# Optimization experiments

Hardware: AMD Instinct MI355X
Metric: run time of the kernel (lower is better)

The kernel has to match this reference:

```python
import jax, jax.numpy as jnp
import numpy as np

B, F, H, W = 1, 6, 20, 26
S = F * H * W            # 3120 tokens
DIM, NH, HD = 1536, 12, 128
C = HD // 2              # 64 rotary channels
T_C = C - 2 * (C // 3)   # 22 temporal channels
H_C = C // 3             # 21
W_C = C // 3             # 21
LOCAL_FRAMES = 4         # local_attn_size (in frames)
SINK_FRAMES = 1          # sink_size (in frames)
EPS = 1e-6
MAX_POS = 1024


def _angle_table(n_ch):
    inv = 1.0 / (10000.0 ** (np.arange(n_ch, dtype=np.float64) / n_ch))
    return np.outer(np.arange(MAX_POS, dtype=np.float64), inv)


def setup_inputs() -> dict:
    key = jax.random.key(0)
    ks = jax.random.split(key, 8)
    sc = 0.02
    ang = np.concatenate([_angle_table(T_C), _angle_table(H_C), _angle_table(W_C)], axis=1)  # [1024, 64]
    return {
        "x": jax.random.normal(ks[0], (B, S, DIM), jnp.float32),
        "seq_lens": jnp.array([S], jnp.int32),
        "grid_sizes": jnp.array([[F, H, W]], jnp.int32),
        "freqs_cos": jnp.asarray(np.cos(ang), jnp.float32),
        "freqs_sin": jnp.asarray(np.sin(ang), jnp.float32),
        "Wq": jax.random.normal(ks[1], (DIM, DIM), jnp.float32) * sc,
        "bq": jnp.zeros((DIM,), jnp.float32),
        "Wk": jax.random.normal(ks[2], (DIM, DIM), jnp.float32) * sc,
        "bk": jnp.zeros((DIM,), jnp.float32),
        "Wv": jax.random.normal(ks[3], (DIM, DIM), jnp.float32) * sc,
        "bv": jnp.zeros((DIM,), jnp.float32),
        "Wo": jax.random.normal(ks[4], (DIM, DIM), jnp.float32) * sc,
        "bo": jnp.zeros((DIM,), jnp.float32),
        "gq": jnp.ones((DIM,), jnp.float32),
        "gk": jnp.ones((DIM,), jnp.float32),
    }


def _rms_norm(x, g):
    # WanRMSNorm: x * rsqrt(mean(x^2) + eps) * weight
    return x * jax.lax.rsqrt(jnp.mean(x * x, axis=-1, keepdims=True) + EPS) * g


def _rope_apply(x, freqs_cos, freqs_sin):
    # x: [B, S, NH, HD]; per-token 3D (f,h,w) rotary on consecutive pairs.
    pos = jnp.arange(S)
    f = pos // (H * W)
    hh = (pos // W) % H
    ww = pos % W
    cos_t, cos_h, cos_w = freqs_cos[:, :T_C], freqs_cos[:, T_C:T_C + H_C], freqs_cos[:, T_C + H_C:]
    sin_t, sin_h, sin_w = freqs_sin[:, :T_C], freqs_sin[:, T_C:T_C + H_C], freqs_sin[:, T_C + H_C:]
    cos = jnp.concatenate([cos_t[f], cos_h[hh], cos_w[ww]], axis=-1)[None, :, None, :]  # [1,S,1,C]
    sin = jnp.concatenate([sin_t[f], sin_h[hh], sin_w[ww]], axis=-1)[None, :, None, :]
    xp = x.reshape(B, S, NH, C, 2)
    xr, xi = xp[..., 0], xp[..., 1]
    out = jnp.stack([xr * cos - xi * sin, xr * sin + xi * cos], axis=-1)
    return out.reshape(B, S, NH, HD)


def _block_mask():
    # frame-causal + local window (in frames) + sink frames: [S, S] bool
    fid = jnp.arange(S) // (H * W)
    fi, fj = fid[:, None], fid[None, :]
    return (fj <= fi) & ((fi - fj < LOCAL_FRAMES) | (fj < SINK_FRAMES))


def reference(x, seq_lens, grid_sizes, freqs_cos, freqs_sin,
              Wq, bq, Wk, bk, Wv, bv, Wo, bo, gq, gk):
    q = _rms_norm(x @ Wq + bq, gq).reshape(B, S, NH, HD)
    k = _rms_norm(x @ Wk + bk, gk).reshape(B, S, NH, HD)
    v = (x @ Wv + bv).reshape(B, S, NH, HD)
    rq = _rope_apply(q, freqs_cos, freqs_sin)
    rk = _rope_apply(k, freqs_cos, freqs_sin)
    scale = 1.0 / jnp.sqrt(jnp.asarray(HD, x.dtype))
    scores = jnp.einsum('bind,bjnd->bnij', rq, rk) * scale  # [B,NH,S,S]
    scores = jnp.where(_block_mask()[None, None], scores, jnp.finfo(scores.dtype).min)
    attn = jax.nn.softmax(scores, axis=-1)
    out = jnp.einsum('bnij,bjnd->bind', attn, v).reshape(B, S, DIM)
    return out @ Wo + bo
```

## Files before the change

kernel.cpp:

```cpp
#include <hip/hip_runtime.h>
#include <hip/hip_bf16.h>
#include <stdint.h>

typedef short v8s __attribute__((ext_vector_type(8)));
typedef float v4f __attribute__((ext_vector_type(4)));
typedef unsigned short u16;

#define S_LEN 3120
#define DIMN 1536
#define NHEAD 12
#define HDIM 128
#define FRM 520
#define NT64 49
#define T64_PH 166
#define TOT64 1992
#define NSTEP32 17
#define SCALE_QK 0.088388347648318447f
#define MAXOFF 12.0f

__device__ __forceinline__ v4f mfma16(v8s a, v8s b, v4f c) {
  return __builtin_amdgcn_mfma_f32_16x16x32_bf16(a, b, c, 0, 0, 0);
}
__device__ __forceinline__ float b2f(u16 u) {
  union { float f; unsigned int i; } x; x.i = ((unsigned int)u) << 16; return x.f;
}
__device__ __forceinline__ u16 f2b(float f) {
  union { float f; unsigned int i; } x; x.f = f;
  unsigned int r = x.i + 0x7FFFu + ((x.i >> 16) & 1u);
  return (u16)(r >> 16);
}
__device__ __forceinline__ void async16(const void* g, void* l) {
  __builtin_amdgcn_global_load_lds(
      (__attribute__((address_space(1))) const void*)g,
      (__attribute__((address_space(3))) void*)l, 16, 0, 0);
}

__global__ void detect_dtype(const u16* __restrict__ w, int* __restrict__ flag) {
  __shared__ int sh;
  int t = threadIdx.x;
  if (t == 0) sh = 0;
  __syncthreads();
  u16 m0 = (u16)(w[2 * t] & 0x7FFF);
  u16 m1 = (u16)(w[2 * t + 1] & 0x7FFF);
  if (m0 >= 0x4480 || m1 >= 0x4480) atomicOr(&sh, 1);
  __syncthreads();
  if (t == 0) *flag = sh;
}

struct PrepArgs {
  const void* tin[4]; u16* tout[4];
  const void* csrc[9]; u16* cdst[9]; int cn[9];
};
__global__ __launch_bounds__(256) void prep(PrepArgs a, const int* __restrict__ flag) {
  int isf = *flag;
  int z = blockIdx.z;
  int t = threadIdx.x;
  if (z < 4) {
    __shared__ u16 tile[32][33];
    const float* inf = (const float*)a.tin[z];
    const u16* inb = (const u16*)a.tin[z];
    u16* out = a.tout[z];
    int tx = t & 31, ty = t >> 5;
    int gr0 = blockIdx.y * 32, gc0 = blockIdx.x * 32;
#pragma unroll
    for (int i = 0; i < 4; ++i) {
      int r = ty + i * 8;
      size_t idx = (size_t)(gr0 + r) * DIMN + gc0 + tx;
      tile[r][tx] = isf ? f2b(inf[idx]) : inb[idx];
    }
    __syncthreads();
#pragma unroll
    for (int i = 0; i < 4; ++i) {
      int r = ty + i * 8;
      out[(size_t)(gc0 + r) * DIMN + gr0 + tx] = tile[tx][r];
    }
  } else {
    int id = z - 4;
    int n = a.cn[id];
    const float* sf = (const float*)a.csrc[id];
    const u16* sb = (const u16*)a.csrc[id];
    u16* d = a.cdst[id];
    int bidx = blockIdx.y * gridDim.x + blockIdx.x;
    int stride = gridDim.x * gridDim.y * 256;
    for (int i = bidx * 256 + t; i < n; i += stride)
      d[i] = isf ? f2b(sf[i]) : sb[i];
  }
}

__global__ __launch_bounds__(256) void transpose16(const u16* __restrict__ in,
                                                   u16* __restrict__ out,
                                                   int rows, int cols) {
  __shared__ u16 tile[32][33];
  int t = threadIdx.x;
  int tx = t & 31, ty = t >> 5;
  int gr0 = blockIdx.y * 32, gc0 = blockIdx.x * 32;
#pragma unroll
  for (int i = 0; i < 4; ++i) {
    int r = ty + i * 8;
    int gr = gr0 + r, gc = gc0 + tx;
    if (gr < rows && gc < cols) tile[r][tx] = in[(size_t)gr * cols + gc];
  }
  __syncthreads();
#pragma unroll
  for (int i = 0; i < 4; ++i) {
    int r = ty + i * 8;
    int orow = gc0 + r, ocol = gr0 + tx;
    if (orow < cols && ocol < rows) out[(size_t)orow * rows + ocol] = tile[tx][r];
  }
}

template <int MT>
__global__ __launch_bounds__(256) void gemm3(
    const u16* __restrict__ A,
    const u16* BT0, const u16* BT1, const u16* BT2,
    const u16* b0, const u16* b1, const u16* b2,
    void* C0, void* C1, void* C2, int M, const int* __restrict__ flag, int dyn) {
  const u16* BT; const u16* bias; void* C;
  if (blockIdx.z == 0)      { BT = BT0; bias = b0; C = C0; }
  else if (blockIdx.z == 1) { BT = BT1; bias = b1; C = C1; }
  else                      { BT = BT2; bias = b2; C = C2; }
  int f32out = dyn ? *flag : 0;
  __shared__ __align__(16) short As[MT * 64];
  __shared__ __align__(16) short Bs[128 * 64];
  int t = threadIdx.x, w = t >> 6, l = t & 63;
  int ln = l & 15, lg = l >> 4;
  int m0 = blockIdx.y * MT, n0 = blockIdx.x * 128;
  int lr = l >> 3;
  int gl = (l & 7) ^ lr;
  constexpr int ACH = MT / 32;
  const u16* gAp[ACH]; short* lAp[ACH];
#pragma unroll
  for (int i = 0; i < ACH; ++i) {
    int c = w * ACH + i;
    int arow = min(m0 + c * 8 + lr, M - 1);
    gAp[i] = A + (size_t)arow * DIMN + gl * 8;
    lAp[i] = As + c * 512;
  }
  const u16* gBp[4]; short* lBp[4];
#pragma unroll
  for (int i = 0; i < 4; ++i) {
    int c = w * 4 + i;
    int brow = n0 + c * 8 + lr;
    gBp[i] = BT + (size_t)brow * DIMN + gl * 8;
    lBp[i] = Bs + c * 512;
  }
  constexpr int NJ = (MT == 128) ? 4 : 2;
  int wm = (MT == 128) ? (w & 1) : 0;
  int wn = (MT == 128) ? (w >> 1) : w;
  int aoff[2][4], boff[2][NJ];
#pragma unroll
  for (int ks = 0; ks < 2; ++ks) {
#pragma unroll
    for (int i = 0; i < 4; ++i) {
      int ar = wm * 64 + i * 16 + ln;
      aoff[ks][i] = ar * 64 + (((ks * 4 + lg) ^ (ar & 7)) * 8);
    }
#pragma unroll
    for (int j = 0; j < NJ; ++j) {
      int br = wn * (NJ * 16) + j * 16 + ln;
      boff[ks][j] = br * 64 + (((ks * 4 + lg) ^ (br & 7)) * 8);
    }
  }
  v4f acc[4][NJ] = {};
  for (int k0 = 0; k0 < DIMN; k0 += 64) {
    __syncthreads();
#pragma unroll
    for (int i = 0; i < ACH; ++i) async16(gAp[i] + k0, lAp[i]);
#pragma unroll
    for (int i = 0; i < 4; ++i) async16(gBp[i] + k0, lBp[i]);
    __syncthreads();
#pragma unroll
    for (int ks = 0; ks < 2; ++ks) {
      v8s af[4], bfr[NJ];
#pragma unroll
      for (int i = 0; i < 4; ++i) af[i] = *(const v8s*)(As + aoff[ks][i]);
#pragma unroll
      for (int j = 0; j < NJ; ++j) bfr[j] = *(const v8s*)(Bs + boff[ks][j]);
#pragma unroll
      for (int i = 0; i < 4; ++i)
#pragma unroll
        for (int j = 0; j < NJ; ++j) acc[i][j] = mfma16(af[i], bfr[j], acc[i][j]);
    }
  }
#pragma unroll
  for (int i = 0; i < 4; ++i) {
    int rb = m0 + wm * 64 + i * 16 + lg * 4;
#pragma unroll
    for (int j = 0; j < NJ; ++j) {
      int col = n0 + wn * (NJ * 16) + j * 16 + ln;
      float bv = b2f(bias[col]);
#pragma unroll
      for (int r = 0; r < 4; ++r) {
        int grow = rb + r;
        if (grow < M) {
          size_t idx = (size_t)grow * DIMN + col;
          float val = acc[i][j][r] + bv;
          if (f32out) ((float*)C)[idx] = val;
          else        ((u16*)C)[idx] = f2b(val);
        }
      }
    }
  }
}

__global__ __launch_bounds__(256) void norm_rope(u16* __restrict__ Q, u16* __restrict__ K,
                                                 const u16* __restrict__ gq,
                                                 const u16* __restrict__ gk,
                                                 const u16* __restrict__ fcos,
                                                 const u16* __restrict__ fsin) {
  int s = blockIdx.x;
  u16* base = (blockIdx.y == 0 ? Q : K) + (size_t)s * DIMN;
  const u16* g = (blockIdx.y == 0) ? gq : gk;
  int t = threadIdx.x;
  int e = t * 6;
  float x[6];
#pragma unroll
  for (int i = 0; i < 6; ++i) x[i] = b2f(base[e + i]);
  float ss = 0.f;
#pragma unroll
  for (int i = 0; i < 6; ++i) ss += x[i] * x[i];
#pragma unroll
  for (int off = 32; off > 0; off >>= 1) ss += __shfl_xor(ss, off);
  __shared__ float red[4];
  if ((t & 63) == 0) red[t >> 6] = ss;
  __syncthreads();
  float tot = red[0] + red[1] + red[2] + red[3];
  float rs = rsqrtf(tot * (1.0f / DIMN) + 1e-6f);
  int f = s / FRM;
  int hh = (s / 26) % 20;
  int ww = s % 26;
#pragma unroll
  for (int u = 0; u < 3; ++u) {
    int e0 = e + 2 * u;
    int c = (e0 & 127) >> 1;
    int p = (c < 22) ? f : ((c < 43) ? hh : ww);
    float co = b2f(fcos[p * 64 + c]);
    float si = b2f(fsin[p * 64 + c]);
    float xr = x[2 * u] * rs * b2f(g[e0]);
    float xi = x[2 * u + 1] * rs * b2f(g[e0 + 1]);
    base[e0]     = f2b(xr * co - xi * si);
    base[e0 + 1] = f2b(xr * si + xi * co);
  }
}

__global__ __launch_bounds__(128) void attn_block(const u16* __restrict__ Q,
                                                  const u16* __restrict__ K,
                                                  const u16* __restrict__ VT,
                                                  u16* __restrict__ Po,
                                                  float* __restrict__ Pl) {
  __shared__ __align__(16) short Ks[32 * 128];
  __shared__ __align__(16) short Vs[128 * 32];
  __shared__ __align__(16) short Pt[2][32 * 40];
  int t = threadIdx.x, w = t >> 6, l = t & 63;
  int ln = l & 15, lg = l >> 4;
  int task = blockIdx.x;
  int head = task / T64_PH, tid = task % T64_PH;
  int tile = 0, frame = 0;
  {
    int acc = 0;
    for (tile = 0; tile < NT64; ++tile) {
      int q0t = tile * 64;
      int f_lo = q0t / FRM;
      int f_hi = min(q0t + 63, S_LEN - 1) / FRM;
      int fstart = max(0, f_lo - 3);
      int sink = fstart > 0;
      int nf = f_hi - fstart + 1 + sink;
      if (tid < acc + nf) {
        int c = tid - acc;
        frame = sink ? (c == 0 ? 0 : fstart + c - 1) : (fstart + c);
        break;
      }
      acc += nf;
    }
  }
  int q0 = tile * 64 + w * 32;
  v8s qf[2][4];
  bool rowok[2][4];
#pragma unroll
  for (int g = 0; g < 2; ++g) {
    int row = min(q0 + g * 16 + ln, S_LEN - 1);
    const u16* qp = Q + (size_t)row * DIMN + head * HDIM + lg * 8;
#pragma unroll
    for (int c = 0; c < 4; ++c) qf[g][c] = *(const v8s*)(qp + c * 32);
#pragma unroll
    for (int r = 0; r < 4; ++r) {
      int qr = q0 + g * 16 + lg * 4 + r;
      int fi = (qr < S_LEN) ? qr / FRM : -1;
      rowok[g][r] = (frame <= fi) && ((fi - frame) < 4 || frame == 0);
    }
  }
  float lsum[2][4] = {};
  v4f o[2][8] = {};
  int kbeg = frame * FRM, kend = kbeg + FRM;
  int kr_i[4], kgl_i[4], vd_i[4], vgl_i[4];
#pragma unroll
  for (int i = 0; i < 4; ++i) {
    int n = (w * 4 + i) * 64 + l;
    kr_i[i] = n >> 4;
    kgl_i[i] = (n & 15) ^ (kr_i[i] & 15);
    vd_i[i] = n >> 2;
    vgl_i[i] = (n & 3) ^ (vd_i[i] & 3);
  }
  const u16* Kb = K + head * HDIM;
  for (int it = 0; it < NSTEP32; ++it) {
    int kb = kbeg + it * 32;
    __syncthreads();
#pragma unroll
    for (int i = 0; i < 4; ++i) {
      int krow = min(kb + kr_i[i], S_LEN - 1);
      async16(Kb + (size_t)krow * DIMN + kgl_i[i] * 8,
              (char*)Ks + (size_t)(w * 4 + i) * 1024);
      async16(VT + (size_t)(head * HDIM + vd_i[i]) * S_LEN + kb + vgl_i[i] * 8,
              (char*)Vs + (size_t)(w * 4 + i) * 1024);
    }
    __syncthreads();
    v4f s[2][2] = {};
#pragma unroll
    for (int kg = 0; kg < 2; ++kg) {
#pragma unroll
      for (int c = 0; c < 4; ++c) {
        v8s kf = *(const v8s*)(&Ks[(kg * 16 + ln) * 128 + (((c * 4 + lg) ^ ln) * 8)]);
        s[0][kg] = mfma16(qf[0][c], kf, s[0][kg]);
        s[1][kg] = mfma16(qf[1][c], kf, s[1][kg]);
      }
    }
#pragma unroll
    for (int g = 0; g < 2; ++g)
#pragma unroll
      for (int kg = 0; kg < 2; ++kg) {
        bool jv = (kb + kg * 16 + ln) < kend;
#pragma unroll
        for (int r = 0; r < 4; ++r) {
          float p = (rowok[g][r] && jv) ? __expf(s[g][kg][r] * SCALE_QK - MAXOFF) : 0.f;
          unsigned int bi = __float_as_uint(p) & 0xffff0000u;
          lsum[g][r] += __uint_as_float(bi);
          Pt[w][(g * 16 + lg * 4 + r) * 40 + kg * 16 + ln] = (u16)(bi >> 16);
        }
      }
    v8s pf0 = *(const v8s*)(&Pt[w][ln * 40 + lg * 8]);
    v8s pf1 = *(const v8s*)(&Pt[w][(16 + ln) * 40 + lg * 8]);
#pragma unroll
    for (int d = 0; d < 8; ++d) {
      int rr = d * 16 + ln;
      v8s vf = *(const v8s*)(&Vs[rr * 32 + ((lg ^ (rr & 3)) * 8)]);
      o[0][d] = mfma16(pf0, vf, o[0][d]);
      o[1][d] = mfma16(pf1, vf, o[1][d]);
    }
  }
#pragma unroll
  for (int g = 0; g < 2; ++g)
#pragma unroll
    for (int r = 0; r < 4; ++r) {
      float v = lsum[g][r];
      v += __shfl_xor(v, 1);
      v += __shfl_xor(v, 2);
      v += __shfl_xor(v, 4);
      v += __shfl_xor(v, 8);
      lsum[g][r] = v;
    }
  size_t pbase = (size_t)task * (64 * 128);
#pragma unroll
  for (int g = 0; g < 2; ++g)
#pragma unroll
    for (int d = 0; d < 8; ++d)
#pragma unroll
      for (int r = 0; r < 4; ++r) {
        int lrow = w * 32 + g * 16 + lg * 4 + r;
        Po[pbase + lrow * 128 + d * 16 + ln] = f2b(o[g][d][r]);
      }
  if (ln == 0) {
#pragma unroll
    for (int g = 0; g < 2; ++g)
#pragma unroll
      for (int r = 0; r < 4; ++r)
        Pl[task * 64 + w * 32 + g * 16 + lg * 4 + r] = lsum[g][r];
  }
}

__global__ __launch_bounds__(256) void attn_combine(const u16* __restrict__ Po,
                                                    const float* __restrict__ Pl,
                                                    u16* __restrict__ Oa) {
  int tile = blockIdx.x, h = blockIdx.y;
  int accv = 0, nf = 0;
  for (int q = 0; q < NT64; ++q) {
    int q0t = q * 64;
    int f_lo = q0t / FRM;
    int f_hi = min(q0t + 63, S_LEN - 1) / FRM;
    int fstart = max(0, f_lo - 3);
    int sink = fstart > 0;
    nf = f_hi - fstart + 1 + sink;
    if (q == tile) break;
    accv += nf;
  }
  int base = h * T64_PH + accv;
  int t = threadIdx.x;
  int row = t >> 2, seg = (t & 3) * 32;
  int grow = tile * 64 + row;
  if (grow >= S_LEN) return;
  float lsum = 0.f;
  float ao[32];
#pragma unroll
  for (int j = 0; j < 32; ++j) ao[j] = 0.f;
  for (int c = 0; c < nf; ++c) {
    int task = base + c;
    lsum += Pl[task * 64 + row];
    const u16* p = Po + (size_t)task * 8192 + row * 128 + seg;
#pragma unroll
    for (int v = 0; v < 4; ++v) {
      v8s x = *(const v8s*)(p + v * 8);
#pragma unroll
      for (int j = 0; j < 8; ++j) ao[v * 8 + j] += b2f((u16)x[j]);
    }
  }
  float inv = 1.0f / lsum;
  u16* dst = Oa + (size_t)grow * DIMN + h * HDIM + seg;
#pragma unroll
  for (int v = 0; v < 4; ++v) {
    v8s res;
#pragma unroll
    for (int j = 0; j < 8; ++j) res[j] = (short)f2b(ao[v * 8 + j] * inv);
    *(v8s*)(dst + v * 8) = res;
  }
}

extern "C" void kernel_launch(void* const* d_in, const int* in_sizes, int n_in,
                              void* d_out, int out_size, void* d_ws, size_t ws_size,
                              hipStream_t stream) {
  (void)n_in; (void)out_size; (void)ws_size;
  int* flag = (int*)d_ws;
  u16* ws = (u16*)d_ws;
  size_t off = 16;
  const size_t SD = (size_t)S_LEN * DIMN;
  const size_t WW = (size_t)DIMN * DIMN;
  const size_t NPO = (size_t)1032 * 128 * 128;
  auto alloc = [&](size_t n) { u16* p = ws + off; off += (n + 7) & ~(size_t)7; return p; };
  u16* Xc  = alloc(SD);
  u16* Fc  = alloc(65536);
  u16* Fs  = alloc(65536);
  u16* bqc = alloc(1536); u16* bkc = alloc(1536); u16* bvc = alloc(1536); u16* boc = alloc(1536);
  u16* gqc = alloc(1536); u16* gkc = alloc(1536);
  u16* Qr = alloc(SD); u16* Kr = alloc(SD); u16* Vr = alloc(SD); u16* Oa = alloc(SD);
  u16* WoT = alloc(WW);
  u16* WqT = alloc(WW); u16* WkT = alloc(WW); u16* WvT = alloc(WW);
  alloc(NPO - 3 * WW);
  float* Pl = (float*)alloc((size_t)TOT64 * 64 * 2);
  u16* Po = WqT;
  u16* VT = Xc;

  detect_dtype<<<1, 256, 0, stream>>>((const u16*)d_in[5], flag);

  PrepArgs pa;
  pa.tin[0] = d_in[5];  pa.tout[0] = WqT;
  pa.tin[1] = d_in[7];  pa.tout[1] = WkT;
  pa.tin[2] = d_in[9];  pa.tout[2] = WvT;
  pa.tin[3] = d_in[11]; pa.tout[3] = WoT;
  const int srcIdx[9] = {0, 3, 4, 6, 8, 10, 12, 13, 14};
  u16* dsts[9] = {Xc, Fc, Fs, bqc, bkc, bvc, boc, gqc, gkc};
  for (int i = 0; i < 9; ++i) {
    pa.csrc[i] = d_in[srcIdx[i]];
    pa.cdst[i] = dsts[i];
    pa.cn[i] = in_sizes[srcIdx[i]];
  }
  dim3 b256(256);
  prep<<<dim3(48, 48, 13), b256, 0, stream>>>(pa, flag);
  gemm3<64><<<dim3(12, 49, 3), b256, 0, stream>>>(Xc, WqT, WkT, WvT, bqc, bkc, bvc,
                                                  Qr, Kr, Vr, S_LEN, flag, 0);
  norm_rope<<<dim3(S_LEN, 2), b256, 0, stream>>>(Qr, Kr, gqc, gkc, Fc, Fs);
  transpose16<<<dim3(48, 98), b256, 0, stream>>>(Vr, VT, S_LEN, DIMN);
  attn_block<<<dim3(TOT64), dim3(128), 0, stream>>>(Qr, Kr, VT, Po, Pl);
  attn_combine<<<dim3(NT64, NHEAD), b256, 0, stream>>>(Po, Pl, Oa);
  gemm3<64><<<dim3(12, 49, 1), b256, 0, stream>>>(Oa, WoT, WoT, WoT, boc, boc, boc,
                                                  d_out, d_out, d_out, S_LEN, flag, 1);
}
```

Before: 373.8 us.

## Double-buffer LDS tiles in projection GEMM and attention block kernels

Both the QKV/output GEMM and the attention block kernel now keep two shared-memory buffers. The next K-slice (or K/V tile) is loaded asynchronously while the current one is consumed, which removes one barrier per iteration and hides global-load latency behind MFMA work. The attention kernel also raises wave priority around its MFMA sections. The cost is double the LDS footprint per block, which may lower occupancy. Correctness also relies on the async copies having completed by the time of the single barrier.

```diff
diff --git a/kernel.cpp b/kernel.cpp
--- a/kernel.cpp
+++ b/kernel.cpp
@@ -120,8 +120,10 @@
   else if (blockIdx.z == 1) { BT = BT1; bias = b1; C = C1; }
   else                      { BT = BT2; bias = b2; C = C2; }
   int f32out = dyn ? *flag : 0;
-  __shared__ __align__(16) short As[MT * 64];
-  __shared__ __align__(16) short Bs[128 * 64];
+  constexpr int ABUF = MT * 64;
+  constexpr int BBUF = 128 * 64;
+  __shared__ __align__(16) short As[2 * ABUF];
+  __shared__ __align__(16) short Bs[2 * BBUF];
   int t = threadIdx.x, w = t >> 6, l = t & 63;
   int ln = l & 15, lg = l >> 4;
   int m0 = blockIdx.y * MT, n0 = blockIdx.x * 128;
@@ -162,25 +164,36 @@
     }
   }
   v4f acc[4][NJ] = {};
-  for (int k0 = 0; k0 < DIMN; k0 += 64) {
-    __syncthreads();
-#pragma unroll
-    for (int i = 0; i < ACH; ++i) async16(gAp[i] + k0, lAp[i]);
-#pragma unroll
-    for (int i = 0; i < 4; ++i) async16(gBp[i] + k0, lBp[i]);
-    __syncthreads();
+  constexpr int NK = DIMN / 64;
+#pragma unroll
+  for (int i = 0; i < ACH; ++i) async16(gAp[i], lAp[i]);
+#pragma unroll
+  for (int i = 0; i < 4; ++i) async16(gBp[i], lBp[i]);
+  __syncthreads();
+  for (int it = 0; it < NK; ++it) {
+    int cur = it & 1;
+    if (it + 1 < NK) {
+      int k0n = (it + 1) * 64;
+      int nb = cur ^ 1;
+#pragma unroll
+      for (int i = 0; i < ACH; ++i) async16(gAp[i] + k0n, lAp[i] + nb * ABUF);
+#pragma unroll
+      for (int i = 0; i < 4; ++i) async16(gBp[i] + k0n, lBp[i] + nb * BBUF);
+    }
+    int ab = cur * ABUF, bb = cur * BBUF;
 #pragma unroll
     for (int ks = 0; ks < 2; ++ks) {
       v8s af[4], bfr[NJ];
 #pragma unroll
-      for (int i = 0; i < 4; ++i) af[i] = *(const v8s*)(As + aoff[ks][i]);
-#pragma unroll
-      for (int j = 0; j < NJ; ++j) bfr[j] = *(const v8s*)(Bs + boff[ks][j]);
+      for (int i = 0; i < 4; ++i) af[i] = *(const v8s*)(As + ab + aoff[ks][i]);
+#pragma unroll
+      for (int j = 0; j < NJ; ++j) bfr[j] = *(const v8s*)(Bs + bb + boff[ks][j]);
 #pragma unroll
       for (int i = 0; i < 4; ++i)
 #pragma unroll
         for (int j = 0; j < NJ; ++j) acc[i][j] = mfma16(af[i], bfr[j], acc[i][j]);
     }
+    __syncthreads();
   }
 #pragma unroll
   for (int i = 0; i < 4; ++i) {
@@ -248,8 +261,8 @@
                                                   const u16* __restrict__ VT,
                                                   u16* __restrict__ Po,
                                                   float* __restrict__ Pl) {
-  __shared__ __align__(16) short Ks[32 * 128];
-  __shared__ __align__(16) short Vs[128 * 32];
+  __shared__ __align__(16) short Ks[2][32 * 128];
+  __shared__ __align__(16) short Vs[2][128 * 32];
   __shared__ __align__(16) short Pt[2][32 * 40];
   int t = threadIdx.x, w = t >> 6, l = t & 63;
   int ln = l & 15, lg = l >> 4;
@@ -302,9 +315,8 @@
     vgl_i[i] = (n & 3) ^ (vd_i[i] & 3);
   }
   const u16* Kb = K + head * HDIM;
-  for (int it = 0; it < NSTEP32; ++it) {
-    int kb = kbeg + it * 32;
-    __syncthreads();
+  {
+    int kb = kbeg;
 #pragma unroll
     for (int i = 0; i < 4; ++i) {
       int krow = min(kb + kr_i[i], S_LEN - 1);
@@ -313,17 +325,35 @@
       async16(VT + (size_t)(head * HDIM + vd_i[i]) * S_LEN + kb + vgl_i[i] * 8,
               (char*)Vs + (size_t)(w * 4 + i) * 1024);
     }
-    __syncthreads();
+  }
+  __syncthreads();
+  for (int it = 0; it < NSTEP32; ++it) {
+    int cur = it & 1;
+    if (it + 1 < NSTEP32) {
+      int kbn = kbeg + (it + 1) * 32;
+      size_t boff = (size_t)(cur ^ 1) * 8192;
+#pragma unroll
+      for (int i = 0; i < 4; ++i) {
+        int krow = min(kbn + kr_i[i], S_LEN - 1);
+        async16(Kb + (size_t)krow * DIMN + kgl_i[i] * 8,
+                (char*)Ks + boff + (size_t)(w * 4 + i) * 1024);
+        async16(VT + (size_t)(head * HDIM + vd_i[i]) * S_LEN + kbn + vgl_i[i] * 8,
+                (char*)Vs + boff + (size_t)(w * 4 + i) * 1024);
+      }
+    }
+    int kb = kbeg + it * 32;
     v4f s[2][2] = {};
+    __builtin_amdgcn_s_setprio(1);
 #pragma unroll
     for (int kg = 0; kg < 2; ++kg) {
 #pragma unroll
       for (int c = 0; c < 4; ++c) {
-        v8s kf = *(const v8s*)(&Ks[(kg * 16 + ln) * 128 + (((c * 4 + lg) ^ ln) * 8)]);
+        v8s kf = *(const v8s*)(&Ks[cur][(kg * 16 + ln) * 128 + (((c * 4 + lg) ^ ln) * 8)]);
         s[0][kg] = mfma16(qf[0][c], kf, s[0][kg]);
         s[1][kg] = mfma16(qf[1][c], kf, s[1][kg]);
       }
     }
+    __builtin_amdgcn_s_setprio(0);
 #pragma unroll
     for (int g = 0; g < 2; ++g)
 #pragma unroll
@@ -339,13 +369,16 @@
       }
     v8s pf0 = *(const v8s*)(&Pt[w][ln * 40 + lg * 8]);
     v8s pf1 = *(const v8s*)(&Pt[w][(16 + ln) * 40 + lg * 8]);
+    __builtin_amdgcn_s_setprio(1);
 #pragma unroll
     for (int d = 0; d < 8; ++d) {
       int rr = d * 16 + ln;
-      v8s vf = *(const v8s*)(&Vs[rr * 32 + ((lg ^ (rr & 3)) * 8)]);
+      v8s vf = *(const v8s*)(&Vs[cur][rr * 32 + ((lg ^ (rr & 3)) * 8)]);
       o[0][d] = mfma16(pf0, vf, o[0][d]);
       o[1][d] = mfma16(pf1, vf, o[1][d]);
     }
+    __builtin_amdgcn_s_setprio(0);
+    __syncthreads();
   }
 #pragma unroll
   for (int g = 0; g < 2; ++g)
```

After: 388.1 us. 3.8% more time.

## Double-buffer K/V tiles in attention block and precompute task map

Applied to the files above, without the earlier changes.

Double-buffers the K and V shared-memory tiles in the attention kernel, issuing the async loads for the next 32-key step before computing on the current one, so there is one barrier per step instead of two. It also adds s_setprio around the MFMA sections and replaces the per-block loop that decoded tile/frame and accv/nf with a constexpr-built constant-memory lookup table. The cost is doubled LDS for K/V, which may lower occupancy. Correctness relies on the async loads having completed at the single end-of-iteration barrier.

```diff
diff --git a/kernel.cpp b/kernel.cpp
--- a/kernel.cpp
+++ b/kernel.cpp
@@ -17,6 +17,35 @@
 #define NSTEP32 17
 #define SCALE_QK 0.088388347648318447f
 #define MAXOFF 12.0f
+
+struct TaskMap {
+  unsigned char tile[T64_PH];
+  unsigned char frame[T64_PH];
+  short accv[NT64];
+  unsigned char nf[NT64];
+};
+constexpr TaskMap make_map() {
+  TaskMap m{};
+  int acc = 0;
+  for (int tile = 0; tile < NT64; ++tile) {
+    int q0t = tile * 64;
+    int f_lo = q0t / FRM;
+    int qhi = q0t + 63 < S_LEN - 1 ? q0t + 63 : S_LEN - 1;
+    int f_hi = qhi / FRM;
+    int fstart = f_lo - 3 > 0 ? f_lo - 3 : 0;
+    int sink = fstart > 0 ? 1 : 0;
+    int nf = f_hi - fstart + 1 + sink;
+    m.accv[tile] = (short)acc;
+    m.nf[tile] = (unsigned char)nf;
+    for (int c = 0; c < nf; ++c) {
+      m.tile[acc + c] = (unsigned char)tile;
+      m.frame[acc + c] = (unsigned char)(sink ? (c == 0 ? 0 : fstart + c - 1) : (fstart + c));
+    }
+    acc += nf;
+  }
+  return m;
+}
+__device__ __constant__ TaskMap TM = make_map();
 
 __device__ __forceinline__ v4f mfma16(v8s a, v8s b, v4f c) {
   return __builtin_amdgcn_mfma_f32_16x16x32_bf16(a, b, c, 0, 0, 0);
@@ -248,31 +277,14 @@
                                                   const u16* __restrict__ VT,
                                                   u16* __restrict__ Po,
                                                   float* __restrict__ Pl) {
-  __shared__ __align__(16) short Ks[32 * 128];
-  __shared__ __align__(16) short Vs[128 * 32];
+  __shared__ __align__(16) short Ks[2][32 * 128];
+  __shared__ __align__(16) short Vs[2][128 * 32];
   __shared__ __align__(16) short Pt[2][32 * 40];
   int t = threadIdx.x, w = t >> 6, l = t & 63;
   int ln = l & 15, lg = l >> 4;
   int task = blockIdx.x;
   int head = task / T64_PH, tid = task % T64_PH;
-  int tile = 0, frame = 0;
-  {
-    int acc = 0;
-    for (tile = 0; tile < NT64; ++tile) {
-      int q0t = tile * 64;
-      int f_lo = q0t / FRM;
-      int f_hi = min(q0t + 63, S_LEN - 1) / FRM;
-      int fstart = max(0, f_lo - 3);
-      int sink = fstart > 0;
-      int nf = f_hi - fstart + 1 + sink;
-      if (tid < acc + nf) {
-        int c = tid - acc;
-        frame = sink ? (c == 0 ? 0 : fstart + c - 1) : (fstart + c);
-        break;
-      }
-      acc += nf;
-    }
-  }
+  int tile = TM.tile[tid], frame = TM.frame[tid];
   int q0 = tile * 64 + w * 32;
   v8s qf[2][4];
   bool rowok[2][4];
@@ -302,9 +314,8 @@
     vgl_i[i] = (n & 3) ^ (vd_i[i] & 3);
   }
   const u16* Kb = K + head * HDIM;
-  for (int it = 0; it < NSTEP32; ++it) {
-    int kb = kbeg + it * 32;
-    __syncthreads();
+  {
+    int kb = kbeg;
 #pragma unroll
     for (int i = 0; i < 4; ++i) {
       int krow = min(kb + kr_i[i], S_LEN - 1);
@@ -313,17 +324,35 @@
       async16(VT + (size_t)(head * HDIM + vd_i[i]) * S_LEN + kb + vgl_i[i] * 8,
               (char*)Vs + (size_t)(w * 4 + i) * 1024);
     }
-    __syncthreads();
+  }
+  __syncthreads();
+  for (int it = 0; it < NSTEP32; ++it) {
+    int cur = it & 1;
+    if (it + 1 < NSTEP32) {
+      int kbn = kbeg + (it + 1) * 32;
+      size_t boff = (size_t)(cur ^ 1) * 8192;
+#pragma unroll
+      for (int i = 0; i < 4; ++i) {
+        int krow = min(kbn + kr_i[i], S_LEN - 1);
+        async16(Kb + (size_t)krow * DIMN + kgl_i[i] * 8,
+                (char*)Ks + boff + (size_t)(w * 4 + i) * 1024);
+        async16(VT + (size_t)(head * HDIM + vd_i[i]) * S_LEN + kbn + vgl_i[i] * 8,
+                (char*)Vs + boff + (size_t)(w * 4 + i) * 1024);
+      }
+    }
+    int kb = kbeg + it * 32;
     v4f s[2][2] = {};
+    __builtin_amdgcn_s_setprio(1);
 #pragma unroll
     for (int kg = 0; kg < 2; ++kg) {
 #pragma unroll
       for (int c = 0; c < 4; ++c) {
-        v8s kf = *(const v8s*)(&Ks[(kg * 16 + ln) * 128 + (((c * 4 + lg) ^ ln) * 8)]);
+        v8s kf = *(const v8s*)(&Ks[cur][(kg * 16 + ln) * 128 + (((c * 4 + lg) ^ ln) * 8)]);
         s[0][kg] = mfma16(qf[0][c], kf, s[0][kg]);
         s[1][kg] = mfma16(qf[1][c], kf, s[1][kg]);
       }
     }
+    __builtin_amdgcn_s_setprio(0);
 #pragma unroll
     for (int g = 0; g < 2; ++g)
 #pragma unroll
@@ -339,13 +368,16 @@
       }
     v8s pf0 = *(const v8s*)(&Pt[w][ln * 40 + lg * 8]);
     v8s pf1 = *(const v8s*)(&Pt[w][(16 + ln) * 40 + lg * 8]);
+    __builtin_amdgcn_s_setprio(1);
 #pragma unroll
     for (int d = 0; d < 8; ++d) {
       int rr = d * 16 + ln;
-      v8s vf = *(const v8s*)(&Vs[rr * 32 + ((lg ^ (rr & 3)) * 8)]);
+      v8s vf = *(const v8s*)(&Vs[cur][rr * 32 + ((lg ^ (rr & 3)) * 8)]);
       o[0][d] = mfma16(pf0, vf, o[0][d]);
       o[1][d] = mfma16(pf1, vf, o[1][d]);
     }
+    __builtin_amdgcn_s_setprio(0);
+    __syncthreads();
   }
 #pragma unroll
   for (int g = 0; g < 2; ++g)
@@ -381,17 +413,7 @@
                                                     const float* __restrict__ Pl,
                                                     u16* __restrict__ Oa) {
   int tile = blockIdx.x, h = blockIdx.y;
-  int accv = 0, nf = 0;
-  for (int q = 0; q < NT64; ++q) {
-    int q0t = q * 64;
-    int f_lo = q0t / FRM;
-    int f_hi = min(q0t + 63, S_LEN - 1) / FRM;
-    int fstart = max(0, f_lo - 3);
-    int sink = fstart > 0;
-    nf = f_hi - fstart + 1 + sink;
-    if (q == tile) break;
-    accv += nf;
-  }
+  int accv = TM.accv[tile], nf = TM.nf[tile];
   int base = h * T64_PH + accv;
   int t = threadIdx.x;
   int row = t >> 2, seg = (t & 3) * 32;
```

Measured after the change: 369.7 us. No clear change (-1.1%).
